# Kernel tuning notes

Measured on AMD Instinct MI355X. Metric: run time of the kernel, lower is better.

## Reference

```python
import jax, jax.numpy as jnp
import numpy as np

SEQ, BATCH, HID, LAYERS = 512, 128, 1024, 4

def setup_inputs() -> dict:
    key = jax.random.key(0)
    ks = jax.random.split(key, 5)
    bound = 1.0 / np.sqrt(HID)  # torch RNNCell init: U(-1/sqrt(H), 1/sqrt(H))
    return {
        "x": jax.random.normal(ks[0], (SEQ, BATCH, HID), dtype=jnp.float32),
        "W_ih": jax.random.uniform(ks[1], (LAYERS, HID, HID), jnp.float32, -bound, bound),
        "W_hh": jax.random.uniform(ks[2], (LAYERS, HID, HID), jnp.float32, -bound, bound),
        "b_ih": jax.random.uniform(ks[3], (LAYERS, HID), jnp.float32, -bound, bound),
        "b_hh": jax.random.uniform(ks[4], (LAYERS, HID), jnp.float32, -bound, bound),
    }

def reference(x, W_ih, W_hh, b_ih, b_hh):
    # x: [T, B, H] time-major. Multi-layer tanh RNN scan.
    L, H = W_ih.shape[0], W_ih.shape[1]
    B = x.shape[1]
    h0 = jnp.zeros((L, B, H), dtype=x.dtype)

    def step(h, x_t):
        # checkpoint path detaches hidden state between steps (no BPTT through carry)
        h = jax.lax.stop_gradient(h)
        cur = x_t
        new_h = []
        for i in range(L):  # small fixed layer loop
            nh = jnp.tanh(cur @ W_ih[i].T + b_ih[i] + h[i] @ W_hh[i].T + b_hh[i])
            new_h.append(nh)
            cur = nh
        return jnp.stack(new_h), cur

    _, outputs = jax.lax.scan(step, h0, x)  # outputs: [T, B, H] (top layer)
    return outputs
```

## Files before the change

### kernel.cpp

```cpp
#include <hip/hip_runtime.h>
#include <stdint.h>

#define T_SEQ 512
#define BATCH 128
#define HID 1024
#define LAYERS 4
#define BK 64
#define LDS_STRIDE 72

typedef __attribute__((ext_vector_type(4))) float f32x4;
typedef __attribute__((ext_vector_type(8))) short s16x8;
typedef __attribute__((ext_vector_type(8))) unsigned short u16x8;

__device__ __forceinline__ unsigned short f2bf(float f) {
    unsigned int x = __builtin_bit_cast(unsigned int, f);
    unsigned int r = (x + 0x7fffu + ((x >> 16) & 1u)) >> 16;
    return (unsigned short)r;
}

__global__ void prep_kernel(const float* __restrict__ Wih, const float* __restrict__ Whh,
                            const float* __restrict__ bih, const float* __restrict__ bhh,
                            unsigned short* __restrict__ Wbf, float* __restrict__ bias) {
    int idx = blockIdx.x * blockDim.x + threadIdx.x;
    const int HH = HID * HID;
    if (idx < LAYERS * HH) {
        int layer = idx / HH;
        int off = idx - layer * HH;
        Wbf[(size_t)layer * 2 * HH + off]      = f2bf(Wih[idx]);
        Wbf[(size_t)layer * 2 * HH + HH + off] = f2bf(Whh[idx]);
    }
    if (idx < LAYERS * HID) bias[idx] = bih[idx] + bhh[idx];
}

__global__ __launch_bounds__(256) void cell_kernel(
        const float* __restrict__ x,
        const unsigned short* __restrict__ Wbf,
        const float* __restrict__ bias,
        unsigned short* __restrict__ hbf,
        float* __restrict__ out,
        int s) {
    const int layer = blockIdx.z;
    const int tt = s - layer;
    if (tt < 0 || tt >= T_SEQ) return;
    const int par = s & 1, prev = par ^ 1;
    const int HH = HID * HID;

    __shared__ unsigned short As[64 * LDS_STRIDE];
    __shared__ unsigned short Bs[64 * LDS_STRIDE];

    const int tid = threadIdx.x;
    const int m0 = blockIdx.y * 64;
    const int n0 = blockIdx.x * 64;
    const int wave = tid >> 6, lane = tid & 63;
    const int wm = (wave >> 1) * 32, wn = (wave & 1) * 32;

    f32x4 acc[2][2];
    for (int f = 0; f < 2; ++f)
        for (int g = 0; g < 2; ++g)
            acc[f][g] = (f32x4){0.f, 0.f, 0.f, 0.f};

    const int srow = tid >> 2;
    const int skq  = (tid & 3) * 16;

    const int nphase = (tt == 0) ? 1 : 2;
    for (int ph = 0; ph < nphase; ++ph) {
        const unsigned short* Wp = Wbf + (size_t)layer * 2 * HH + (size_t)ph * HH;
        const float* xsrc = nullptr;
        const unsigned short* hsrc = nullptr;
        if (ph == 0) {
            if (layer == 0) xsrc = x + (size_t)tt * BATCH * HID;
            else hsrc = hbf + (size_t)((layer - 1) * 2 + prev) * BATCH * HID;
        } else {
            hsrc = hbf + (size_t)(layer * 2 + prev) * BATCH * HID;
        }

        for (int k0 = 0; k0 < HID; k0 += BK) {
            const unsigned short* wptr = Wp + (size_t)(n0 + srow) * HID + k0 + skq;
            u16x8 breg0 = *(const u16x8*)wptr;
            u16x8 breg1 = *(const u16x8*)(wptr + 8);

            u16x8 areg0, areg1;
            if (xsrc) {
                const float* ap = xsrc + (size_t)(m0 + srow) * HID + k0 + skq;
                f32x4 f0 = *(const f32x4*)(ap);
                f32x4 f1 = *(const f32x4*)(ap + 4);
                f32x4 f2 = *(const f32x4*)(ap + 8);
                f32x4 f3 = *(const f32x4*)(ap + 12);
                for (int j = 0; j < 4; ++j) {
                    areg0[j]     = f2bf(f0[j]);
                    areg0[4 + j] = f2bf(f1[j]);
                    areg1[j]     = f2bf(f2[j]);
                    areg1[4 + j] = f2bf(f3[j]);
                }
            } else {
                const unsigned short* ap = hsrc + (size_t)(m0 + srow) * HID + k0 + skq;
                areg0 = *(const u16x8*)(ap);
                areg1 = *(const u16x8*)(ap + 8);
            }

            __syncthreads();
            *(u16x8*)&Bs[srow * LDS_STRIDE + skq]     = breg0;
            *(u16x8*)&Bs[srow * LDS_STRIDE + skq + 8] = breg1;
            *(u16x8*)&As[srow * LDS_STRIDE + skq]     = areg0;
            *(u16x8*)&As[srow * LDS_STRIDE + skq + 8] = areg1;
            __syncthreads();

            const int l15 = lane & 15;
            for (int kk = 0; kk < 2; ++kk) {
                const int kb = kk * 32 + ((lane >> 4) << 3);
                s16x8 a0 = *(const s16x8*)&As[(wm + 0  + l15) * LDS_STRIDE + kb];
                s16x8 a1 = *(const s16x8*)&As[(wm + 16 + l15) * LDS_STRIDE + kb];
                s16x8 b0 = *(const s16x8*)&Bs[(wn + 0  + l15) * LDS_STRIDE + kb];
                s16x8 b1 = *(const s16x8*)&Bs[(wn + 16 + l15) * LDS_STRIDE + kb];
                acc[0][0] = __builtin_amdgcn_mfma_f32_16x16x32_bf16(a0, b0, acc[0][0], 0, 0, 0);
                acc[0][1] = __builtin_amdgcn_mfma_f32_16x16x32_bf16(a0, b1, acc[0][1], 0, 0, 0);
                acc[1][0] = __builtin_amdgcn_mfma_f32_16x16x32_bf16(a1, b0, acc[1][0], 0, 0, 0);
                acc[1][1] = __builtin_amdgcn_mfma_f32_16x16x32_bf16(a1, b1, acc[1][1], 0, 0, 0);
            }
        }
    }

    const int col = lane & 15;
    const int rq = (lane >> 4) << 2;
    unsigned short* hdst = hbf + (size_t)(layer * 2 + par) * BATCH * HID;
    for (int f = 0; f < 2; ++f) {
        for (int g = 0; g < 2; ++g) {
            const int gn = n0 + wn + g * 16 + col;
            const float bv = bias[layer * HID + gn];
            for (int r = 0; r < 4; ++r) {
                const int gm = m0 + wm + f * 16 + rq + r;
                float v = tanhf(acc[f][g][r] + bv);
                hdst[(size_t)gm * HID + gn] = f2bf(v);
                if (layer == LAYERS - 1)
                    out[((size_t)tt * BATCH + gm) * HID + gn] = v;
            }
        }
    }
}

extern "C" void kernel_launch(void* const* d_in, const int* in_sizes, int n_in,
                              void* d_out, int out_size, void* d_ws, size_t ws_size,
                              hipStream_t stream) {
    const float* x   = (const float*)d_in[0];
    const float* Wih = (const float*)d_in[1];
    const float* Whh = (const float*)d_in[2];
    const float* bih = (const float*)d_in[3];
    const float* bhh = (const float*)d_in[4];
    float* out = (float*)d_out;

    unsigned short* Wbf = (unsigned short*)d_ws;
    float* bias = (float*)((char*)d_ws + (size_t)LAYERS * 2 * HID * HID * 2);
    unsigned short* hbf = (unsigned short*)((char*)d_ws + (size_t)LAYERS * 2 * HID * HID * 2 + 64 * 1024);

    {
        int total = LAYERS * HID * HID;
        int blocks = (total + 255) / 256;
        hipLaunchKernelGGL(prep_kernel, dim3(blocks), dim3(256), 0, stream,
                           Wih, Whh, bih, bhh, Wbf, bias);
    }

    for (int s = 0; s < T_SEQ + LAYERS - 1; ++s) {
        hipLaunchKernelGGL(cell_kernel, dim3(16, 2, 4), dim3(256), 0, stream,
                           x, Wbf, bias, hbf, out, s);
    }
}
```

Measured before the change: 16.03 ms.

## Replace per-step launches with persistent cooperative kernel keeping weights in LDS

Swaps the 515 per-stage kernel launches for one cooperative persistent kernel of 256 blocks. Each block converts its 32-column slice of W_ih and W_hh to bf16 once and keeps it resident in LDS. Stages are separated by a custom grid barrier built from flag atomics and a go word. The input and recurrent GEMMs run on separate wave pairs and are combined through an LDS reduction. This removes launch overhead and the repeated weight reloads from global memory, at the cost of a centralized spin barrier on every step and a dependence on all 256 blocks being co-resident.

```diff
diff --git a/kernel.cpp b/kernel.cpp
--- a/kernel.cpp
+++ b/kernel.cpp
@@ -5,136 +5,221 @@
 #define BATCH 128
 #define HID 1024
 #define LAYERS 4
-#define BK 64
-#define LDS_STRIDE 72
+#define NSTAGES (T_SEQ + LAYERS - 1)
+#define NBLK 256
+#define WSTRIDE 1032
+#define SMEM_BYTES (2*32*WSTRIDE*2 + 8192 + 128)
 
 typedef __attribute__((ext_vector_type(4))) float f32x4;
 typedef __attribute__((ext_vector_type(8))) short s16x8;
 typedef __attribute__((ext_vector_type(8))) unsigned short u16x8;
+typedef __attribute__((ext_vector_type(4))) unsigned short u16x4;
 
 __device__ __forceinline__ unsigned short f2bf(float f) {
     unsigned int x = __builtin_bit_cast(unsigned int, f);
-    unsigned int r = (x + 0x7fffu + ((x >> 16) & 1u)) >> 16;
-    return (unsigned short)r;
+    return (unsigned short)((x + 0x7fffu + ((x >> 16) & 1u)) >> 16);
 }
 
-__global__ void prep_kernel(const float* __restrict__ Wih, const float* __restrict__ Whh,
-                            const float* __restrict__ bih, const float* __restrict__ bhh,
-                            unsigned short* __restrict__ Wbf, float* __restrict__ bias) {
-    int idx = blockIdx.x * blockDim.x + threadIdx.x;
-    const int HH = HID * HID;
-    if (idx < LAYERS * HH) {
-        int layer = idx / HH;
-        int off = idx - layer * HH;
-        Wbf[(size_t)layer * 2 * HH + off]      = f2bf(Wih[idx]);
-        Wbf[(size_t)layer * 2 * HH + HH + off] = f2bf(Whh[idx]);
+__global__ __launch_bounds__(256, 1) void rnn_kernel(
+        const float* __restrict__ x,
+        const float* __restrict__ Wih,
+        const float* __restrict__ Whh,
+        const float* __restrict__ bih,
+        const float* __restrict__ bhh,
+        float* __restrict__ out,
+        unsigned int* __restrict__ sync,
+        unsigned short* __restrict__ hbf)
+{
+    extern __shared__ char smem[];
+    unsigned short* Wlds = (unsigned short*)smem;
+    float* redbuf = (float*)(smem + 2 * 32 * WSTRIDE * 2);
+    float* bias_s = (float*)(smem + 2 * 32 * WSTRIDE * 2 + 8192);
+
+    const int bid = blockIdx.x;
+    const int wid = ((bid & 7) << 5) | (bid >> 3);
+    const int layer = wid >> 6;
+    const int mh = (wid >> 5) & 1;
+    const int ns = wid & 31;
+    const int n0 = ns * 32;
+    const int m0 = mh * 64;
+
+    const int tid = threadIdx.x;
+    const int wave = tid >> 6;
+    const int lane = tid & 63;
+    const int ph = wave >> 1;
+    const int mrow = (wave & 1) * 32;
+    const int l15 = lane & 15;
+    const int kq8 = (lane >> 4) << 3;
+
+    {
+        const int p = tid >> 7;
+        const int col = (tid >> 2) & 31;
+        const int kq = (tid & 3) * 256;
+        const float* __restrict__ wsrc =
+            (p == 0 ? Wih : Whh) + (size_t)layer * HID * HID + (size_t)(n0 + col) * HID + kq;
+        unsigned short* dst = Wlds + (p * 32 + col) * WSTRIDE + kq;
+        #pragma unroll 4
+        for (int i = 0; i < 64; ++i) {
+            f32x4 v = *(const f32x4*)(wsrc + i * 4);
+            u16x4 o;
+            o[0] = f2bf(v[0]); o[1] = f2bf(v[1]); o[2] = f2bf(v[2]); o[3] = f2bf(v[3]);
+            *(u16x4*)(dst + i * 4) = o;
+        }
+        if (tid < 32)
+            bias_s[tid] = bih[layer * HID + n0 + tid] + bhh[layer * HID + n0 + tid];
     }
-    if (idx < LAYERS * HID) bias[idx] = bih[idx] + bhh[idx];
-}
-
-__global__ __launch_bounds__(256) void cell_kernel(
-        const float* __restrict__ x,
-        const unsigned short* __restrict__ Wbf,
-        const float* __restrict__ bias,
-        unsigned short* __restrict__ hbf,
-        float* __restrict__ out,
-        int s) {
-    const int layer = blockIdx.z;
-    const int tt = s - layer;
-    if (tt < 0 || tt >= T_SEQ) return;
-    const int par = s & 1, prev = par ^ 1;
-    const int HH = HID * HID;
-
-    __shared__ unsigned short As[64 * LDS_STRIDE];
-    __shared__ unsigned short Bs[64 * LDS_STRIDE];
-
-    const int tid = threadIdx.x;
-    const int m0 = blockIdx.y * 64;
-    const int n0 = blockIdx.x * 64;
-    const int wave = tid >> 6, lane = tid & 63;
-    const int wm = (wave >> 1) * 32, wn = (wave & 1) * 32;
-
-    f32x4 acc[2][2];
-    for (int f = 0; f < 2; ++f)
-        for (int g = 0; g < 2; ++g)
-            acc[f][g] = (f32x4){0.f, 0.f, 0.f, 0.f};
-
-    const int srow = tid >> 2;
-    const int skq  = (tid & 3) * 16;
-
-    const int nphase = (tt == 0) ? 1 : 2;
-    for (int ph = 0; ph < nphase; ++ph) {
-        const unsigned short* Wp = Wbf + (size_t)layer * 2 * HH + (size_t)ph * HH;
-        const float* xsrc = nullptr;
-        const unsigned short* hsrc = nullptr;
-        if (ph == 0) {
-            if (layer == 0) xsrc = x + (size_t)tt * BATCH * HID;
-            else hsrc = hbf + (size_t)((layer - 1) * 2 + prev) * BATCH * HID;
-        } else {
-            hsrc = hbf + (size_t)(layer * 2 + prev) * BATCH * HID;
-        }
-
-        for (int k0 = 0; k0 < HID; k0 += BK) {
-            const unsigned short* wptr = Wp + (size_t)(n0 + srow) * HID + k0 + skq;
-            u16x8 breg0 = *(const u16x8*)wptr;
-            u16x8 breg1 = *(const u16x8*)(wptr + 8);
-
-            u16x8 areg0, areg1;
-            if (xsrc) {
-                const float* ap = xsrc + (size_t)(m0 + srow) * HID + k0 + skq;
-                f32x4 f0 = *(const f32x4*)(ap);
-                f32x4 f1 = *(const f32x4*)(ap + 4);
-                f32x4 f2 = *(const f32x4*)(ap + 8);
-                f32x4 f3 = *(const f32x4*)(ap + 12);
-                for (int j = 0; j < 4; ++j) {
-                    areg0[j]     = f2bf(f0[j]);
-                    areg0[4 + j] = f2bf(f1[j]);
-                    areg1[j]     = f2bf(f2[j]);
-                    areg1[4 + j] = f2bf(f3[j]);
+    __syncthreads();
+
+    unsigned int* flags = sync;
+    unsigned int* go = sync + 256;
+
+    const int bbase0 = (ph * 32 + l15) * WSTRIDE + kq8;
+    const int bbase1 = (ph * 32 + 16 + l15) * WSTRIDE + kq8;
+
+    for (int s = 0; s < NSTAGES; ++s) {
+        const int tt = s - layer;
+        if (tt >= 0 && tt < T_SEQ) {
+            const int par = s & 1, prev = par ^ 1;
+            f32x4 acc00 = {0.f,0.f,0.f,0.f}, acc01 = {0.f,0.f,0.f,0.f};
+            f32x4 acc10 = {0.f,0.f,0.f,0.f}, acc11 = {0.f,0.f,0.f,0.f};
+
+            if (!(ph == 1 && tt == 0)) {
+                if (ph == 0 && layer == 0) {
+                    const float* __restrict__ a0p =
+                        x + ((size_t)tt * BATCH + m0 + mrow + l15) * HID + kq8;
+                    const float* __restrict__ a1p = a0p + 16 * HID;
+                    f32x4 pf[8][2][2];
+                    #pragma unroll
+                    for (int p = 0; p < 8; ++p) {
+                        pf[p][0][0] = *(const f32x4*)(a0p + p * 32);
+                        pf[p][0][1] = *(const f32x4*)(a0p + p * 32 + 4);
+                        pf[p][1][0] = *(const f32x4*)(a1p + p * 32);
+                        pf[p][1][1] = *(const f32x4*)(a1p + p * 32 + 4);
+                    }
+                    #pragma unroll
+                    for (int ks = 0; ks < 32; ++ks) {
+                        const int sl = ks & 7;
+                        u16x8 av0, av1;
+                        #pragma unroll
+                        for (int j = 0; j < 4; ++j) {
+                            av0[j]     = f2bf(pf[sl][0][0][j]);
+                            av0[4 + j] = f2bf(pf[sl][0][1][j]);
+                            av1[j]     = f2bf(pf[sl][1][0][j]);
+                            av1[4 + j] = f2bf(pf[sl][1][1][j]);
+                        }
+                        if (ks + 8 < 32) {
+                            pf[sl][0][0] = *(const f32x4*)(a0p + (ks + 8) * 32);
+                            pf[sl][0][1] = *(const f32x4*)(a0p + (ks + 8) * 32 + 4);
+                            pf[sl][1][0] = *(const f32x4*)(a1p + (ks + 8) * 32);
+                            pf[sl][1][1] = *(const f32x4*)(a1p + (ks + 8) * 32 + 4);
+                        }
+                        s16x8 b0 = *(const s16x8*)(Wlds + bbase0 + ks * 32);
+                        s16x8 b1 = *(const s16x8*)(Wlds + bbase1 + ks * 32);
+                        acc00 = __builtin_amdgcn_mfma_f32_16x16x32_bf16((s16x8)av0, b0, acc00, 0, 0, 0);
+                        acc01 = __builtin_amdgcn_mfma_f32_16x16x32_bf16((s16x8)av0, b1, acc01, 0, 0, 0);
+                        acc10 = __builtin_amdgcn_mfma_f32_16x16x32_bf16((s16x8)av1, b0, acc10, 0, 0, 0);
+                        acc11 = __builtin_amdgcn_mfma_f32_16x16x32_bf16((s16x8)av1, b1, acc11, 0, 0, 0);
+                    }
+                } else {
+                    const unsigned short* __restrict__ src = (ph == 0)
+                        ? hbf + (size_t)((layer - 1) * 2 + prev) * BATCH * HID
+                        : hbf + (size_t)(layer * 2 + prev) * BATCH * HID;
+                    const unsigned short* __restrict__ a0p =
+                        src + (size_t)(m0 + mrow + l15) * HID + kq8;
+                    const unsigned short* __restrict__ a1p = a0p + 16 * HID;
+                    u16x8 ab[8][2];
+                    #pragma unroll
+                    for (int p = 0; p < 8; ++p) {
+                        ab[p][0] = *(const u16x8*)(a0p + p * 32);
+                        ab[p][1] = *(const u16x8*)(a1p + p * 32);
+                    }
+                    #pragma unroll
+                    for (int ks = 0; ks < 32; ++ks) {
+                        const int sl = ks & 7;
+                        s16x8 a0 = (s16x8)ab[sl][0];
+                        s16x8 a1 = (s16x8)ab[sl][1];
+                        if (ks + 8 < 32) {
+                            ab[sl][0] = *(const u16x8*)(a0p + (ks + 8) * 32);
+                            ab[sl][1] = *(const u16x8*)(a1p + (ks + 8) * 32);
+                        }
+                        s16x8 b0 = *(const s16x8*)(Wlds + bbase0 + ks * 32);
+                        s16x8 b1 = *(const s16x8*)(Wlds + bbase1 + ks * 32);
+                        acc00 = __builtin_amdgcn_mfma_f32_16x16x32_bf16(a0, b0, acc00, 0, 0, 0);
+                        acc01 = __builtin_amdgcn_mfma_f32_16x16x32_bf16(a0, b1, acc01, 0, 0, 0);
+                        acc10 = __builtin_amdgcn_mfma_f32_16x16x32_bf16(a1, b0, acc10, 0, 0, 0);
+                        acc11 = __builtin_amdgcn_mfma_f32_16x16x32_bf16(a1, b1, acc11, 0, 0, 0);
+                    }
                 }
-            } else {
-                const unsigned short* ap = hsrc + (size_t)(m0 + srow) * HID + k0 + skq;
-                areg0 = *(const u16x8*)(ap);
-                areg1 = *(const u16x8*)(ap + 8);
             }
 
             __syncthreads();
-            *(u16x8*)&Bs[srow * LDS_STRIDE + skq]     = breg0;
-            *(u16x8*)&Bs[srow * LDS_STRIDE + skq + 8] = breg1;
-            *(u16x8*)&As[srow * LDS_STRIDE + skq]     = areg0;
-            *(u16x8*)&As[srow * LDS_STRIDE + skq + 8] = areg1;
+            if (ph == 1) {
+                float* rb = redbuf + (wave & 1) * 1024;
+                *(f32x4*)(rb + (0 * 64 + lane) * 4) = acc00;
+                *(f32x4*)(rb + (1 * 64 + lane) * 4) = acc01;
+                *(f32x4*)(rb + (2 * 64 + lane) * 4) = acc10;
+                *(f32x4*)(rb + (3 * 64 + lane) * 4) = acc11;
+            }
             __syncthreads();
-
-            const int l15 = lane & 15;
-            for (int kk = 0; kk < 2; ++kk) {
-                const int kb = kk * 32 + ((lane >> 4) << 3);
-                s16x8 a0 = *(const s16x8*)&As[(wm + 0  + l15) * LDS_STRIDE + kb];
-                s16x8 a1 = *(const s16x8*)&As[(wm + 16 + l15) * LDS_STRIDE + kb];
-                s16x8 b0 = *(const s16x8*)&Bs[(wn + 0  + l15) * LDS_STRIDE + kb];
-                s16x8 b1 = *(const s16x8*)&Bs[(wn + 16 + l15) * LDS_STRIDE + kb];
-                acc[0][0] = __builtin_amdgcn_mfma_f32_16x16x32_bf16(a0, b0, acc[0][0], 0, 0, 0);
-                acc[0][1] = __builtin_amdgcn_mfma_f32_16x16x32_bf16(a0, b1, acc[0][1], 0, 0, 0);
-                acc[1][0] = __builtin_amdgcn_mfma_f32_16x16x32_bf16(a1, b0, acc[1][0], 0, 0, 0);
-                acc[1][1] = __builtin_amdgcn_mfma_f32_16x16x32_bf16(a1, b1, acc[1][1], 0, 0, 0);
-            }
-        }
-    }
-
-    const int col = lane & 15;
-    const int rq = (lane >> 4) << 2;
-    unsigned short* hdst = hbf + (size_t)(layer * 2 + par) * BATCH * HID;
-    for (int f = 0; f < 2; ++f) {
-        for (int g = 0; g < 2; ++g) {
-            const int gn = n0 + wn + g * 16 + col;
-            const float bv = bias[layer * HID + gn];
-            for (int r = 0; r < 4; ++r) {
-                const int gm = m0 + wm + f * 16 + rq + r;
-                float v = tanhf(acc[f][g][r] + bv);
-                hdst[(size_t)gm * HID + gn] = f2bf(v);
-                if (layer == LAYERS - 1)
-                    out[((size_t)tt * BATCH + gm) * HID + gn] = v;
-            }
-        }
+            if (ph == 0) {
+                const float* rb = redbuf + (wave & 1) * 1024;
+                acc00 += *(const f32x4*)(rb + (0 * 64 + lane) * 4);
+                acc01 += *(const f32x4*)(rb + (1 * 64 + lane) * 4);
+                acc10 += *(const f32x4*)(rb + (2 * 64 + lane) * 4);
+                acc11 += *(const f32x4*)(rb + (3 * 64 + lane) * 4);
+                const float bv0 = bias_s[l15];
+                const float bv1 = bias_s[16 + l15];
+                unsigned short* __restrict__ hdst =
+                    hbf + (size_t)(layer * 2 + par) * BATCH * HID;
+                const int rbase = m0 + mrow + ((lane >> 4) << 2);
+                #pragma unroll
+                for (int mf = 0; mf < 2; ++mf) {
+                    f32x4 aN0 = mf ? acc10 : acc00;
+                    f32x4 aN1 = mf ? acc11 : acc01;
+                    #pragma unroll
+                    for (int r = 0; r < 4; ++r) {
+                        const int gm = rbase + mf * 16 + r;
+                        float v0 = tanhf(aN0[r] + bv0);
+                        float v1 = tanhf(aN1[r] + bv1);
+                        hdst[(size_t)gm * HID + n0 + l15]      = f2bf(v0);
+                        hdst[(size_t)gm * HID + n0 + 16 + l15] = f2bf(v1);
+                        if (layer == LAYERS - 1) {
+                            out[((size_t)tt * BATCH + gm) * HID + n0 + l15]      = v0;
+                            out[((size_t)tt * BATCH + gm) * HID + n0 + 16 + l15] = v1;
+                        }
+                    }
+                }
+            }
+        }
+
+        __syncthreads();
+        const unsigned int g = (unsigned int)(s + 1);
+        if (tid == 0) {
+            __threadfence();
+            __hip_atomic_store(&flags[bid], g, __ATOMIC_RELAXED, __HIP_MEMORY_SCOPE_AGENT);
+        }
+        if (bid == 0) {
+            if (tid < 64) {
+                for (;;) {
+                    bool ok = true;
+                    #pragma unroll
+                    for (int j = 0; j < 4; ++j)
+                        ok = ok && (__hip_atomic_load(&flags[tid + j * 64], __ATOMIC_RELAXED,
+                                                      __HIP_MEMORY_SCOPE_AGENT) >= g);
+                    if (__all((int)ok)) break;
+                    __builtin_amdgcn_s_sleep(1);
+                }
+            }
+            __syncthreads();
+            if (tid == 0)
+                __hip_atomic_store(go, g, __ATOMIC_RELAXED, __HIP_MEMORY_SCOPE_AGENT);
+        }
+        if (tid == 0) {
+            while (__hip_atomic_load(go, __ATOMIC_RELAXED, __HIP_MEMORY_SCOPE_AGENT) < g)
+                __builtin_amdgcn_s_sleep(1);
+            __threadfence();
+        }
+        __syncthreads();
     }
 }
 
@@ -148,19 +233,20 @@
     const float* bhh = (const float*)d_in[4];
     float* out = (float*)d_out;
 
-    unsigned short* Wbf = (unsigned short*)d_ws;
-    float* bias = (float*)((char*)d_ws + (size_t)LAYERS * 2 * HID * HID * 2);
-    unsigned short* hbf = (unsigned short*)((char*)d_ws + (size_t)LAYERS * 2 * HID * HID * 2 + 64 * 1024);
-
-    {
-        int total = LAYERS * HID * HID;
-        int blocks = (total + 255) / 256;
-        hipLaunchKernelGGL(prep_kernel, dim3(blocks), dim3(256), 0, stream,
-                           Wih, Whh, bih, bhh, Wbf, bias);
+    unsigned int* sync = (unsigned int*)d_ws;
+    unsigned short* hbf = (unsigned short*)((char*)d_ws + 4096);
+
+    static bool attr_done = false;
+    if (!attr_done) {
+        hipFuncSetAttribute((const void*)rnn_kernel,
+                            hipFuncAttributeMaxDynamicSharedMemorySize, SMEM_BYTES);
+        attr_done = true;
     }
 
-    for (int s = 0; s < T_SEQ + LAYERS - 1; ++s) {
-        hipLaunchKernelGGL(cell_kernel, dim3(16, 2, 4), dim3(256), 0, stream,
-                           x, Wbf, bias, hbf, out, s);
-    }
+    hipMemsetAsync(d_ws, 0, 4096, stream);
+
+    void* args[] = {(void*)&x, (void*)&Wih, (void*)&Whh, (void*)&bih, (void*)&bhh,
+                    (void*)&out, (void*)&sync, (void*)&hbf};
+    hipLaunchCooperativeKernel((const void*)rnn_kernel, dim3(NBLK), dim3(256),
+                               args, SMEM_BYTES, stream);
 }
```

Measured after the change: 14.66 ms. 8.5% less time.
